# Kernel tuning notes

Measured on AMD Instinct MI355X. Metric: run time of the kernel, lower is better.

The kernel has to match this reference:

```python
import jax, jax.numpy as jnp
import numpy as np

N_NODES = 50000
N_EDGES = 640000
IN_FEATS = 128
HID = 128


def setup_inputs() -> dict:
    key = jax.random.key(0)
    ks = jax.random.split(key, 8)
    x = jax.random.normal(ks[0], (N_NODES, IN_FEATS), dtype=jnp.float32)
    src = jax.random.randint(ks[1], (N_EDGES,), 0, N_NODES, dtype=jnp.int32)
    dst = jax.random.randint(ks[2], (N_EDGES,), 0, N_NODES, dtype=jnp.int32)
    s1 = 1.0 / np.sqrt(IN_FEATS)
    s2 = 1.0 / np.sqrt(HID)
    W1 = jax.random.normal(ks[3], (IN_FEATS, HID), dtype=jnp.float32) * s1
    b1 = jnp.zeros((HID,), dtype=jnp.float32)
    W2 = jax.random.normal(ks[4], (HID, HID), dtype=jnp.float32) * s2
    b2 = jnp.zeros((HID,), dtype=jnp.float32)
    Wr = jax.random.normal(ks[5], (HID, 2), dtype=jnp.float32) * s2
    br = jnp.zeros((2,), dtype=jnp.float32)
    return {"x": x, "src": src, "dst": dst, "W1": W1, "b1": b1,
            "W2": W2, "b2": b2, "Wr": Wr, "br": br}


def _degree_norm(idx, n):
    # D^{-1/2}, with 0 for zero-degree nodes (DGL sets inf -> 0)
    deg = jax.ops.segment_sum(jnp.ones(idx.shape[0], jnp.float32), idx, num_segments=n)
    return jnp.where(deg > 0, jax.lax.rsqrt(jnp.maximum(deg, 1.0)), 0.0)


def _graph_conv(h, W, b, src, dst, norm_out, norm_in, n):
    # DGL GraphConv, norm='both': out = D_in^{-1/2} A D_out^{-1/2} (h W) + b
    hW = (h * norm_out[:, None]) @ W          # [N, hid]
    agg = jax.ops.segment_sum(hW[src], dst, num_segments=n)  # gather+scatter over edges
    return agg * norm_in[:, None] + b


def reference(x, src, dst, W1, b1, W2, b2, Wr, br):
    n = x.shape[0]
    norm_out = _degree_norm(src, n)  # source-side out-degree norm
    norm_in = _degree_norm(dst, n)   # dest-side in-degree norm
    h = jax.nn.relu(_graph_conv(x, W1, b1, src, dst, norm_out, norm_in, n))
    h = jax.nn.relu(_graph_conv(h, W2, b2, src, dst, norm_out, norm_in, n))
    hg = jnp.mean(h, axis=0, keepdims=True)  # [1, hid]
    return hg @ Wr + br                      # [1, 2]
```

## Files before the change

kernel.cpp:

```cpp
#include <hip/hip_runtime.h>
#include <hip/hip_bf16.h>

#define FEAT 128
#define RBITS 12
#define RSIZE 4096
#define NCHUNK 64

typedef __attribute__((ext_vector_type(8))) short short8;
typedef __attribute__((ext_vector_type(4))) short short4v;
typedef __attribute__((ext_vector_type(4))) float f32x4;

__device__ __forceinline__ ushort f2bf(float f) {
    union { float f; unsigned u; } v; v.f = f;
    unsigned u = v.u;
    unsigned r = 0x7fffu + ((u >> 16) & 1u);
    return (ushort)((u + r) >> 16);
}
__device__ __forceinline__ float bf2f(short s) {
    union { unsigned u; float f; } v;
    v.u = ((unsigned)(ushort)s) << 16;
    return v.f;
}

__global__ __launch_bounds__(256)
void hist_kernel(const int* __restrict__ src, const int* __restrict__ dst,
                 unsigned* __restrict__ partial, int E, int CS)
{
    __shared__ unsigned hist[RSIZE];
    const int c = blockIdx.x, p = blockIdx.y, job = blockIdx.z;
    const int* __restrict__ idx = job ? dst : src;
    for (int r = threadIdx.x; r < RSIZE; r += 256) hist[r] = 0;
    __syncthreads();
    const int e0 = c * CS, e1 = min(E, e0 + CS);
    for (int e = e0 + threadIdx.x; e < e1; e += 256) {
        int v = idx[e];
        if ((v >> RBITS) == p) atomicAdd(&hist[v & (RSIZE - 1)], 1u);
    }
    __syncthreads();
    unsigned* out = partial +
        (((size_t)job * gridDim.y + p) * NCHUNK + c) * RSIZE;
    for (int r = threadIdx.x; r < RSIZE; r += 256) out[r] = hist[r];
}

__global__ __launch_bounds__(256)
void merge_kernel(unsigned* __restrict__ partialOut, unsigned* __restrict__ partialIn,
                  int* __restrict__ cntIn, float* __restrict__ normOut,
                  float* __restrict__ normIn, int N)
{
    int n = blockIdx.x * 256 + threadIdx.x;
    if (n >= N) return;
    const int p = n >> RBITS, r = n & (RSIZE - 1);
    const size_t base = (size_t)p * NCHUNK * RSIZE + r;
    unsigned so = 0;
#pragma unroll 8
    for (int c = 0; c < NCHUNK; ++c) so += partialOut[base + (size_t)c * RSIZE];
    unsigned off = 0;
#pragma unroll 8
    for (int c = 0; c < NCHUNK; ++c) {
        size_t i = base + (size_t)c * RSIZE;
        unsigned t = partialIn[i];
        partialIn[i] = off;
        off += t;
    }
    cntIn[n]   = (int)off;
    normIn[n]  = off ? rsqrtf((float)off) : 0.0f;
    normOut[n] = so  ? rsqrtf((float)so)  : 0.0f;
}

__global__ __launch_bounds__(256)
void scan1_kernel(const int* __restrict__ cnt, int* __restrict__ blockSums, int N)
{
    __shared__ int sh[256];
    int i = blockIdx.x * 256 + threadIdx.x;
    sh[threadIdx.x] = (i < N) ? cnt[i] : 0;
    __syncthreads();
    for (int off = 128; off > 0; off >>= 1) {
        if (threadIdx.x < off) sh[threadIdx.x] += sh[threadIdx.x + off];
        __syncthreads();
    }
    if (threadIdx.x == 0) blockSums[blockIdx.x] = sh[0];
}

__global__ __launch_bounds__(256)
void rowstart_kernel(const int* __restrict__ cntIn, const int* __restrict__ blockSums,
                     int* __restrict__ rowStart, int N, int NB, int E)
{
    __shared__ int bs[256];
    __shared__ int bse[256];
    __shared__ int sh[256];
    const int t = threadIdx.x;
    int bv = (t < NB) ? blockSums[t] : 0;
    bs[t] = bv;
    __syncthreads();
    for (int off = 1; off < 256; off <<= 1) {
        int u = (t >= off) ? bs[t - off] : 0;
        __syncthreads();
        bs[t] += u;
        __syncthreads();
    }
    bse[t] = bs[t] - bv;
    __syncthreads();

    const int i = blockIdx.x * 256 + t;
    int v = (i < N) ? cntIn[i] : 0;
    sh[t] = v;
    __syncthreads();
    for (int off = 1; off < 256; off <<= 1) {
        int u = (t >= off) ? sh[t - off] : 0;
        __syncthreads();
        sh[t] += u;
        __syncthreads();
    }
    if (i < N) rowStart[i] = bse[blockIdx.x] + sh[t] - v;
    if (blockIdx.x == 0 && t == 0) rowStart[N] = E;
}

__global__ __launch_bounds__(256)
void fill_kernel(const int* __restrict__ src, const int* __restrict__ dst,
                 const int* __restrict__ rowStart, const unsigned* __restrict__ chunkOff,
                 int* __restrict__ csrSrc, int N, int E, int CS)
{
    __shared__ unsigned cursor[RSIZE];
    const int c = blockIdx.x, p = blockIdx.y;
    const unsigned* co = chunkOff + ((size_t)p * NCHUNK + c) * RSIZE;
    for (int r = threadIdx.x; r < RSIZE; r += 256) {
        int n = (p << RBITS) + r;
        cursor[r] = (n < N) ? (unsigned)rowStart[n] + co[r] : 0u;
    }
    __syncthreads();
    const int e0 = c * CS, e1 = min(E, e0 + CS);
    for (int e = e0 + threadIdx.x; e < e1; e += 256) {
        int d = dst[e];
        if ((d >> RBITS) == p) {
            unsigned pos = atomicAdd(&cursor[d & (RSIZE - 1)], 1u);
            csrSrc[pos] = src[e];
        }
    }
}

template<bool F32IN>
__global__ __launch_bounds__(256)
void gemm_mfma_kernel(const void* __restrict__ Ain, const float* __restrict__ W,
                      const float* __restrict__ scale, ushort* __restrict__ C,
                      int M, int nStrips)
{
    __shared__ ushort WT[128 * 132];
    __shared__ ushort As[64 * 132];
    __shared__ float  sScale[64];

    const int tid  = threadIdx.x;
    const int wv   = tid >> 6;
    const int lane = tid & 63;
    const int rowHalf = wv >> 1;
    const int colHalf = wv & 1;
    const int l15  = lane & 15;
    const int quad = lane >> 4;

    for (int it = 0; it < 16; ++it) {
        int fid = tid + (it << 8);
        int k   = fid >> 5;
        int c4  = (fid & 31) << 2;
        float4 w = *(const float4*)(W + (size_t)k * FEAT + c4);
        WT[(c4 + 0) * 132 + k] = f2bf(w.x);
        WT[(c4 + 1) * 132 + k] = f2bf(w.y);
        WT[(c4 + 2) * 132 + k] = f2bf(w.z);
        WT[(c4 + 3) * 132 + k] = f2bf(w.w);
    }
    __syncthreads();

    short8 bfrag[4][4];
#pragma unroll
    for (int ct = 0; ct < 4; ++ct) {
        int col = colHalf * 64 + ct * 16 + l15;
#pragma unroll
        for (int kst = 0; kst < 4; ++kst) {
            int k = kst * 32 + quad * 8;
            short4v lo = *(const short4v*)&WT[col * 132 + k];
            short4v hi = *(const short4v*)&WT[col * 132 + k + 4];
            bfrag[ct][kst] = __builtin_shufflevector(lo, hi, 0, 1, 2, 3, 4, 5, 6, 7);
        }
    }

    for (int s = blockIdx.x; s < nStrips; s += gridDim.x) {
        const int row0 = s << 6;
        __syncthreads();

#pragma unroll
        for (int it = 0; it < 4; ++it) {
            int fid = tid + (it << 8);
            int r   = fid >> 4;
            int seg = (fid & 15) << 3;
            int grow = row0 + r;
            short4v lo = {0, 0, 0, 0}, hi = {0, 0, 0, 0};
            if (grow < M) {
                if (F32IN) {
                    const float* pa = (const float*)Ain + (size_t)grow * FEAT + seg;
                    float4 u0 = *(const float4*)(pa);
                    float4 u1 = *(const float4*)(pa + 4);
                    lo[0] = (short)f2bf(u0.x); lo[1] = (short)f2bf(u0.y);
                    lo[2] = (short)f2bf(u0.z); lo[3] = (short)f2bf(u0.w);
                    hi[0] = (short)f2bf(u1.x); hi[1] = (short)f2bf(u1.y);
                    hi[2] = (short)f2bf(u1.z); hi[3] = (short)f2bf(u1.w);
                } else {
                    const ushort* pa = (const ushort*)Ain + (size_t)grow * FEAT + seg;
                    lo = *(const short4v*)(pa);
                    hi = *(const short4v*)(pa + 4);
                }
            }
            *(short4v*)&As[r * 132 + seg]     = lo;
            *(short4v*)&As[r * 132 + seg + 4] = hi;
        }
        if (tid < 64) {
            int grow = row0 + tid;
            sScale[tid] = (grow < M) ? scale[grow] : 0.0f;
        }
        __syncthreads();

        f32x4 acc[2][4] = {};
#pragma unroll
        for (int kst = 0; kst < 4; ++kst) {
            int k = kst * 32 + quad * 8;
            short8 af[2];
#pragma unroll
            for (int rt = 0; rt < 2; ++rt) {
                int row = rowHalf * 32 + rt * 16 + l15;
                short4v lo = *(const short4v*)&As[row * 132 + k];
                short4v hi = *(const short4v*)&As[row * 132 + k + 4];
                af[rt] = __builtin_shufflevector(lo, hi, 0, 1, 2, 3, 4, 5, 6, 7);
            }
#pragma unroll
            for (int rt = 0; rt < 2; ++rt)
#pragma unroll
                for (int ct = 0; ct < 4; ++ct)
                    acc[rt][ct] = __builtin_amdgcn_mfma_f32_16x16x32_bf16(
                        af[rt], bfrag[ct][kst], acc[rt][ct], 0, 0, 0);
        }

#pragma unroll
        for (int rt = 0; rt < 2; ++rt) {
            int rbase = rowHalf * 32 + rt * 16 + quad * 4;
#pragma unroll
            for (int reg = 0; reg < 4; ++reg) {
                int rl = rbase + reg;
                int grow = row0 + rl;
                if (grow < M) {
                    float sc = sScale[rl];
#pragma unroll
                    for (int ct = 0; ct < 4; ++ct) {
                        int col = colHalf * 64 + ct * 16 + l15;
                        C[(size_t)grow * FEAT + col] = f2bf(acc[rt][ct][reg] * sc);
                    }
                }
            }
        }
    }
}

__global__ __launch_bounds__(256)
void gather_kernel(const ushort* __restrict__ t, const int* __restrict__ rowStart,
                   const int* __restrict__ csrSrc, const float* __restrict__ normIn,
                   const float* __restrict__ bias, ushort* __restrict__ out, int N)
{
    const int hw   = threadIdx.x >> 5;
    const int lane = threadIdx.x & 31;
    const int node = blockIdx.x * 8 + hw;
    if (node >= N) return;
    const int s = rowStart[node];
    const int e = rowStart[node + 1];
    float a0 = 0.f, a1 = 0.f, a2 = 0.f, a3 = 0.f;
    for (int base = s; base < e; base += 32) {
        const int m = min(32, e - base);
        int idx = (base + lane < e) ? csrSrc[base + lane] : 0;
        int j = 0;
        for (; j + 4 <= m; j += 4) {
            int s0 = __shfl(idx, j,     32);
            int s1 = __shfl(idx, j + 1, 32);
            int s2 = __shfl(idx, j + 2, 32);
            int s3 = __shfl(idx, j + 3, 32);
            short4v v0 = *(const short4v*)(t + (size_t)s0 * FEAT + lane * 4);
            short4v v1 = *(const short4v*)(t + (size_t)s1 * FEAT + lane * 4);
            short4v v2 = *(const short4v*)(t + (size_t)s2 * FEAT + lane * 4);
            short4v v3 = *(const short4v*)(t + (size_t)s3 * FEAT + lane * 4);
            a0 += bf2f(v0[0]) + bf2f(v1[0]) + bf2f(v2[0]) + bf2f(v3[0]);
            a1 += bf2f(v0[1]) + bf2f(v1[1]) + bf2f(v2[1]) + bf2f(v3[1]);
            a2 += bf2f(v0[2]) + bf2f(v1[2]) + bf2f(v2[2]) + bf2f(v3[2]);
            a3 += bf2f(v0[3]) + bf2f(v1[3]) + bf2f(v2[3]) + bf2f(v3[3]);
        }
        for (; j < m; ++j) {
            int srcn = __shfl(idx, j, 32);
            short4v v = *(const short4v*)(t + (size_t)srcn * FEAT + lane * 4);
            a0 += bf2f(v[0]); a1 += bf2f(v[1]); a2 += bf2f(v[2]); a3 += bf2f(v[3]);
        }
    }
    float ni = normIn[node];
    float4 b = *(const float4*)(bias + lane * 4);
    short4v o;
    o[0] = (short)f2bf(fmaxf(fmaf(a0, ni, b.x), 0.0f));
    o[1] = (short)f2bf(fmaxf(fmaf(a1, ni, b.y), 0.0f));
    o[2] = (short)f2bf(fmaxf(fmaf(a2, ni, b.z), 0.0f));
    o[3] = (short)f2bf(fmaxf(fmaf(a3, ni, b.w), 0.0f));
    *(short4v*)(out + (size_t)node * FEAT + lane * 4) = o;
}

__global__ __launch_bounds__(256)
void colreduce_kernel(const ushort* __restrict__ h2, float* __restrict__ colsum, int N)
{
    const int c  = threadIdx.x & 127;
    const int rg = threadIdx.x >> 7;
    const int r0 = blockIdx.x * 256;
    const int rEnd = min(r0 + 256, N);
    float acc = 0.0f;
    for (int r = r0 + rg; r < rEnd; r += 2)
        acc += bf2f(h2[(size_t)r * FEAT + c]);
    __shared__ float sh[256];
    sh[threadIdx.x] = acc;
    __syncthreads();
    if (rg == 0) unsafeAtomicAdd(&colsum[c], sh[c] + sh[128 + c]);
}

__global__ __launch_bounds__(128)
void final_kernel(const float* __restrict__ colsum, const float* __restrict__ Wr,
                  const float* __restrict__ br, float* __restrict__ out, float invN)
{
    __shared__ float s0[128], s1[128];
    int j = threadIdx.x;
    float hg = colsum[j] * invN;
    s0[j] = hg * Wr[2 * j + 0];
    s1[j] = hg * Wr[2 * j + 1];
    __syncthreads();
    for (int off = 64; off > 0; off >>= 1) {
        if (j < off) { s0[j] += s0[j + off]; s1[j] += s1[j + off]; }
        __syncthreads();
    }
    if (j == 0) {
        out[0] = s0[0] + br[0];
        out[1] = s1[0] + br[1];
    }
}

extern "C" void kernel_launch(void* const* d_in, const int* in_sizes, int n_in,
                              void* d_out, int out_size, void* d_ws, size_t ws_size,
                              hipStream_t stream)
{
    const float* x   = (const float*)d_in[0];
    const int*   src = (const int*)d_in[1];
    const int*   dst = (const int*)d_in[2];
    const float* W1  = (const float*)d_in[3];
    const float* b1  = (const float*)d_in[4];
    const float* W2  = (const float*)d_in[5];
    const float* b2  = (const float*)d_in[6];
    const float* Wr  = (const float*)d_in[7];
    const float* br  = (const float*)d_in[8];
    float* out = (float*)d_out;

    const int N = in_sizes[0] / FEAT;
    const int E = in_sizes[1];
    const int NP = ((N + 255) / 256) * 256;
    const int NB = (N + 255) / 256;
    const int P  = (N + RSIZE - 1) / RSIZE;
    const int CS = (E + NCHUNK - 1) / NCHUNK;

    char* p = (char*)d_ws;
    unsigned* partial   = (unsigned*)p;  p += (size_t)2 * P * NCHUNK * RSIZE * 4;
    float*  colsum    = (float*)p;       p += 256 * 4;
    int*    blockSums = (int*)p;         p += 256 * 4;
    int*    cntIn     = (int*)p;         p += (size_t)NP * 4;
    float*  normOut   = (float*)p;       p += (size_t)NP * 4;
    float*  normIn    = (float*)p;       p += (size_t)NP * 4;
    int*    rowStart  = (int*)p;         p += (size_t)(NP + 64) * 4;
    int*    csrSrc    = (int*)p;         p += (size_t)E * 4;
    ushort* bufT      = (ushort*)p;      p += (size_t)N * FEAT * 2;
    ushort* bufH      = (ushort*)p;      p += (size_t)N * FEAT * 2;

    unsigned* partialOut = partial;
    unsigned* partialIn  = partial + (size_t)P * NCHUNK * RSIZE;

    hipMemsetAsync(colsum, 0, 256 * 4, stream);

    hist_kernel<<<dim3(NCHUNK, P, 2), 256, 0, stream>>>(src, dst, partial, E, CS);
    merge_kernel<<<NB, 256, 0, stream>>>(partialOut, partialIn, cntIn, normOut, normIn, N);
    scan1_kernel<<<NB, 256, 0, stream>>>(cntIn, blockSums, N);
    rowstart_kernel<<<NB, 256, 0, stream>>>(cntIn, blockSums, rowStart, N, NB, E);
    fill_kernel<<<dim3(NCHUNK, P), 256, 0, stream>>>(src, dst, rowStart, partialIn, csrSrc, N, E, CS);

    const int nStrips = (N + 63) / 64;
    const int gathBlocks = (N + 7) / 8;

    gemm_mfma_kernel<true><<<256, 256, 0, stream>>>((const void*)x, W1, normOut, bufT, N, nStrips);
    gather_kernel<<<gathBlocks, 256, 0, stream>>>(bufT, rowStart, csrSrc, normIn, b1, bufH, N);

    gemm_mfma_kernel<false><<<256, 256, 0, stream>>>((const void*)bufH, W2, normOut, bufT, N, nStrips);
    gather_kernel<<<gathBlocks, 256, 0, stream>>>(bufT, rowStart, csrSrc, normIn, b2, bufH, N);

    colreduce_kernel<<<NB, 256, 0, stream>>>(bufH, colsum, N);
    final_kernel<<<1, 128, 0, stream>>>(colsum, Wr, br, out, 1.0f / (float)N);
}
```

Baseline: 258.3 us.

## Build CSR with global atomic degree counts and atomic-cursor fill

Replaces the partitioned shared-memory histogram, merge and chunk-offset CSR build with a simpler path. One kernel counts in- and out-degrees with global atomics. The scan kernel also computes both norms, and rowstart seeds a cursor array. The fill then scatters source indices through atomic cursor increments. This removes the repeated per-partition passes over the edge arrays and the large partial-count buffers, and drops one launch. In exchange, edge order within each CSR row becomes nondeterministic, so the float summation order in the gather varies between runs.

```diff
diff --git a/kernel.cpp b/kernel.cpp
--- a/kernel.cpp
+++ b/kernel.cpp
@@ -2,9 +2,6 @@
 #include <hip/hip_bf16.h>
 
 #define FEAT 128
-#define RBITS 12
-#define RSIZE 4096
-#define NCHUNK 64
 
 typedef __attribute__((ext_vector_type(8))) short short8;
 typedef __attribute__((ext_vector_type(4))) short short4v;
@@ -23,56 +20,40 @@
 }
 
 __global__ __launch_bounds__(256)
-void hist_kernel(const int* __restrict__ src, const int* __restrict__ dst,
-                 unsigned* __restrict__ partial, int E, int CS)
-{
-    __shared__ unsigned hist[RSIZE];
-    const int c = blockIdx.x, p = blockIdx.y, job = blockIdx.z;
-    const int* __restrict__ idx = job ? dst : src;
-    for (int r = threadIdx.x; r < RSIZE; r += 256) hist[r] = 0;
-    __syncthreads();
-    const int e0 = c * CS, e1 = min(E, e0 + CS);
-    for (int e = e0 + threadIdx.x; e < e1; e += 256) {
-        int v = idx[e];
-        if ((v >> RBITS) == p) atomicAdd(&hist[v & (RSIZE - 1)], 1u);
-    }
-    __syncthreads();
-    unsigned* out = partial +
-        (((size_t)job * gridDim.y + p) * NCHUNK + c) * RSIZE;
-    for (int r = threadIdx.x; r < RSIZE; r += 256) out[r] = hist[r];
-}
-
-__global__ __launch_bounds__(256)
-void merge_kernel(unsigned* __restrict__ partialOut, unsigned* __restrict__ partialIn,
-                  int* __restrict__ cntIn, float* __restrict__ normOut,
-                  float* __restrict__ normIn, int N)
-{
-    int n = blockIdx.x * 256 + threadIdx.x;
-    if (n >= N) return;
-    const int p = n >> RBITS, r = n & (RSIZE - 1);
-    const size_t base = (size_t)p * NCHUNK * RSIZE + r;
-    unsigned so = 0;
-#pragma unroll 8
-    for (int c = 0; c < NCHUNK; ++c) so += partialOut[base + (size_t)c * RSIZE];
-    unsigned off = 0;
-#pragma unroll 8
-    for (int c = 0; c < NCHUNK; ++c) {
-        size_t i = base + (size_t)c * RSIZE;
-        unsigned t = partialIn[i];
-        partialIn[i] = off;
-        off += t;
-    }
-    cntIn[n]   = (int)off;
-    normIn[n]  = off ? rsqrtf((float)off) : 0.0f;
-    normOut[n] = so  ? rsqrtf((float)so)  : 0.0f;
-}
-
-__global__ __launch_bounds__(256)
-void scan1_kernel(const int* __restrict__ cnt, int* __restrict__ blockSums, int N)
+void deg_kernel(const int* __restrict__ src, const int* __restrict__ dst,
+                int* __restrict__ degOut, int* __restrict__ degIn, int E)
+{
+    int i = (blockIdx.x * 256 + threadIdx.x) * 4;
+    if (i + 4 <= E) {
+        int4 s = *(const int4*)(src + i);
+        int4 d = *(const int4*)(dst + i);
+        atomicAdd(&degOut[s.x], 1); atomicAdd(&degOut[s.y], 1);
+        atomicAdd(&degOut[s.z], 1); atomicAdd(&degOut[s.w], 1);
+        atomicAdd(&degIn[d.x], 1);  atomicAdd(&degIn[d.y], 1);
+        atomicAdd(&degIn[d.z], 1);  atomicAdd(&degIn[d.w], 1);
+    } else {
+        for (int e = i; e < E; ++e) {
+            atomicAdd(&degOut[src[e]], 1);
+            atomicAdd(&degIn[dst[e]], 1);
+        }
+    }
+}
+
+__global__ __launch_bounds__(256)
+void scan_norm_kernel(const int* __restrict__ degIn, const int* __restrict__ degOut,
+                      int* __restrict__ blockSums, float* __restrict__ normIn,
+                      float* __restrict__ normOut, int N)
 {
     __shared__ int sh[256];
     int i = blockIdx.x * 256 + threadIdx.x;
-    sh[threadIdx.x] = (i < N) ? cnt[i] : 0;
+    int d = 0;
+    if (i < N) {
+        d = degIn[i];
+        int dOut = degOut[i];
+        normIn[i]  = d    ? rsqrtf((float)d)    : 0.0f;
+        normOut[i] = dOut ? rsqrtf((float)dOut) : 0.0f;
+    }
+    sh[threadIdx.x] = d;
     __syncthreads();
     for (int off = 128; off > 0; off >>= 1) {
         if (threadIdx.x < off) sh[threadIdx.x] += sh[threadIdx.x + off];
@@ -83,7 +64,8 @@
 
 __global__ __launch_bounds__(256)
 void rowstart_kernel(const int* __restrict__ cntIn, const int* __restrict__ blockSums,
-                     int* __restrict__ rowStart, int N, int NB, int E)
+                     int* __restrict__ rowStart, int* __restrict__ cursor,
+                     int N, int NB, int E)
 {
     __shared__ int bs[256];
     __shared__ int bse[256];
@@ -111,29 +93,32 @@
         sh[t] += u;
         __syncthreads();
     }
-    if (i < N) rowStart[i] = bse[blockIdx.x] + sh[t] - v;
+    if (i < N) {
+        int rs = bse[blockIdx.x] + sh[t] - v;
+        rowStart[i] = rs;
+        cursor[i]   = rs;
+    }
     if (blockIdx.x == 0 && t == 0) rowStart[N] = E;
 }
 
 __global__ __launch_bounds__(256)
-void fill_kernel(const int* __restrict__ src, const int* __restrict__ dst,
-                 const int* __restrict__ rowStart, const unsigned* __restrict__ chunkOff,
-                 int* __restrict__ csrSrc, int N, int E, int CS)
-{
-    __shared__ unsigned cursor[RSIZE];
-    const int c = blockIdx.x, p = blockIdx.y;
-    const unsigned* co = chunkOff + ((size_t)p * NCHUNK + c) * RSIZE;
-    for (int r = threadIdx.x; r < RSIZE; r += 256) {
-        int n = (p << RBITS) + r;
-        cursor[r] = (n < N) ? (unsigned)rowStart[n] + co[r] : 0u;
-    }
-    __syncthreads();
-    const int e0 = c * CS, e1 = min(E, e0 + CS);
-    for (int e = e0 + threadIdx.x; e < e1; e += 256) {
-        int d = dst[e];
-        if ((d >> RBITS) == p) {
-            unsigned pos = atomicAdd(&cursor[d & (RSIZE - 1)], 1u);
-            csrSrc[pos] = src[e];
+void fill_atomic_kernel(const int* __restrict__ src, const int* __restrict__ dst,
+                        int* __restrict__ cursor, int* __restrict__ csrSrc, int E)
+{
+    int i = (blockIdx.x * 256 + threadIdx.x) * 4;
+    if (i + 4 <= E) {
+        int4 s = *(const int4*)(src + i);
+        int4 d = *(const int4*)(dst + i);
+        int p0 = atomicAdd(&cursor[d.x], 1);
+        int p1 = atomicAdd(&cursor[d.y], 1);
+        int p2 = atomicAdd(&cursor[d.z], 1);
+        int p3 = atomicAdd(&cursor[d.w], 1);
+        csrSrc[p0] = s.x; csrSrc[p1] = s.y;
+        csrSrc[p2] = s.z; csrSrc[p3] = s.w;
+    } else {
+        for (int e = i; e < E; ++e) {
+            int p = atomicAdd(&cursor[dst[e]], 1);
+            csrSrc[p] = src[e];
         }
     }
 }
@@ -357,31 +342,28 @@
     const int E = in_sizes[1];
     const int NP = ((N + 255) / 256) * 256;
     const int NB = (N + 255) / 256;
-    const int P  = (N + RSIZE - 1) / RSIZE;
-    const int CS = (E + NCHUNK - 1) / NCHUNK;
 
     char* p = (char*)d_ws;
-    unsigned* partial   = (unsigned*)p;  p += (size_t)2 * P * NCHUNK * RSIZE * 4;
-    float*  colsum    = (float*)p;       p += 256 * 4;
-    int*    blockSums = (int*)p;         p += 256 * 4;
-    int*    cntIn     = (int*)p;         p += (size_t)NP * 4;
-    float*  normOut   = (float*)p;       p += (size_t)NP * 4;
-    float*  normIn    = (float*)p;       p += (size_t)NP * 4;
-    int*    rowStart  = (int*)p;         p += (size_t)(NP + 64) * 4;
-    int*    csrSrc    = (int*)p;         p += (size_t)E * 4;
-    ushort* bufT      = (ushort*)p;      p += (size_t)N * FEAT * 2;
-    ushort* bufH      = (ushort*)p;      p += (size_t)N * FEAT * 2;
-
-    unsigned* partialOut = partial;
-    unsigned* partialIn  = partial + (size_t)P * NCHUNK * RSIZE;
-
-    hipMemsetAsync(colsum, 0, 256 * 4, stream);
-
-    hist_kernel<<<dim3(NCHUNK, P, 2), 256, 0, stream>>>(src, dst, partial, E, CS);
-    merge_kernel<<<NB, 256, 0, stream>>>(partialOut, partialIn, cntIn, normOut, normIn, N);
-    scan1_kernel<<<NB, 256, 0, stream>>>(cntIn, blockSums, N);
-    rowstart_kernel<<<NB, 256, 0, stream>>>(cntIn, blockSums, rowStart, N, NB, E);
-    fill_kernel<<<dim3(NCHUNK, P), 256, 0, stream>>>(src, dst, rowStart, partialIn, csrSrc, N, E, CS);
+    float* colsum    = (float*)p;        p += 256 * 4;
+    int*   degOut    = (int*)p;          p += (size_t)NP * 4;
+    int*   degIn     = (int*)p;          p += (size_t)NP * 4;
+    int*   blockSums = (int*)p;          p += 256 * 4;
+    float* normOut   = (float*)p;        p += (size_t)NP * 4;
+    float* normIn    = (float*)p;        p += (size_t)NP * 4;
+    int*   rowStart  = (int*)p;          p += (size_t)(NP + 64) * 4;
+    int*   cursor    = (int*)p;          p += (size_t)NP * 4;
+    int*   csrSrc    = (int*)p;          p += (size_t)E * 4;
+    ushort* bufT     = (ushort*)p;       p += (size_t)N * FEAT * 2;
+    ushort* bufH     = (ushort*)p;       p += (size_t)N * FEAT * 2;
+
+    hipMemsetAsync(colsum, 0, (256 + 2 * (size_t)NP) * 4, stream);
+
+    const int EB = (E / 4 + 255) / 256;
+
+    deg_kernel<<<EB, 256, 0, stream>>>(src, dst, degOut, degIn, E);
+    scan_norm_kernel<<<NB, 256, 0, stream>>>(degIn, degOut, blockSums, normIn, normOut, N);
+    rowstart_kernel<<<NB, 256, 0, stream>>>(degIn, blockSums, rowStart, cursor, N, NB, E);
+    fill_atomic_kernel<<<EB, 256, 0, stream>>>(src, dst, cursor, csrSrc, E);
 
     const int nStrips = (N + 63) / 64;
     const int gathBlocks = (N + 7) / 8;
```

Measured after the change: 289.8 us. 1.12x slower.
